# Performance work log

Measured on AMD Instinct MI355X. Metric: run time of the kernel, lower is better.

## Reference

```python
import jax, jax.numpy as jnp
import numpy as np

BETA = 0.5
THR = 1.0

@jax.custom_vjp
def spike(u):
    # heaviside fire; surrogate ATan gradient (snntorch default, alpha=2)
    return (u > 0.0).astype(u.dtype)

def _spike_fwd(u):
    return spike(u), u

def _spike_bwd(u, g):
    return (g / (1.0 + (jnp.pi * u) ** 2),)

spike.defvjp(_spike_fwd, _spike_bwd)

def setup_inputs() -> dict:
    key = jax.random.key(0)
    k = jax.random.split(key, 5)
    T, B, NI, NH, NO = 100, 65536, 2, 10, 4
    x = jax.random.normal(k[0], (T, B, NI), dtype=jnp.float32)
    # PyTorch Linear init: U(-1/sqrt(fan_in), 1/sqrt(fan_in))
    W1 = jax.random.uniform(k[1], (NH, NI), jnp.float32, -1/np.sqrt(NI), 1/np.sqrt(NI))
    b1 = jax.random.uniform(k[2], (NH,), jnp.float32, -1/np.sqrt(NI), 1/np.sqrt(NI))
    W2 = jax.random.uniform(k[3], (NO, NH), jnp.float32, -1/np.sqrt(NH), 1/np.sqrt(NH))
    b2 = jax.random.uniform(k[4], (NO,), jnp.float32, -1/np.sqrt(NH), 1/np.sqrt(NH))
    return {"x": x, "W1": W1, "b1": b1, "W2": W2, "b2": b2}

def _lif(mem_prev, syn):
    # snntorch Leaky, reset_mechanism='subtract':
    # reset computed from PRE-update membrane, detached
    reset = jax.lax.stop_gradient((mem_prev > THR).astype(syn.dtype))
    mem = BETA * mem_prev + syn - reset * THR
    spk = spike(mem - THR)
    return spk, mem

def reference(x, W1, b1, W2, b2):
    T, B = x.shape[0], x.shape[1]
    mem1_0 = jnp.zeros((B, W1.shape[0]), x.dtype)
    mem2_0 = jnp.zeros((B, W2.shape[0]), x.dtype)

    def step(carry, xt):
        mem1, mem2 = carry
        syn1 = xt @ W1.T + b1            # [B, NH]
        spk1, mem1 = _lif(mem1, syn1)
        syn2 = spk1 @ W2.T + b2          # [B, NO]
        spk2, mem2 = _lif(mem2, syn2)
        return (mem1, mem2), (spk1, mem1, spk2, mem2)

    _, (spk1_rec, mem1_rec, spk2_rec, mem2_rec) = jax.lax.scan(step, (mem1_0, mem2_0), x)
    return spk1_rec, mem1_rec, spk2_rec, mem2_rec
```

## Files before the change

### kernel.cpp

```cpp
#include <hip/hip_runtime.h>
#include <stdint.h>

#define T_STEPS 100
#define BATCH   65536
#define NI      2
#define NH      10
#define NO      4
#define KCH     10
#define TC      10

typedef float vf2 __attribute__((ext_vector_type(2)));
typedef float vf4 __attribute__((ext_vector_type(4)));

#define LOAD_WEIGHTS                                                        \
    float w1[NH][NI], bb1[NH], w2[NO][NH], bb2[NO];                         \
    _Pragma("unroll") for (int h = 0; h < NH; ++h) {                        \
        w1[h][0] = W1[h * NI + 0];                                          \
        w1[h][1] = W1[h * NI + 1];                                          \
        bb1[h]   = b1[h];                                                   \
    }                                                                       \
    _Pragma("unroll") for (int o = 0; o < NO; ++o) {                        \
        _Pragma("unroll") for (int h = 0; h < NH; ++h)                      \
            w2[o][h] = W2[o * NH + h];                                      \
        bb2[o] = b2[o];                                                     \
    }

__device__ __forceinline__ void lif_step(
    const float x0, const float x1,
    const float w1[NH][NI], const float bb1[NH],
    const float w2[NO][NH], const float bb2[NO],
    float m1[NH], float m2[NO], float spk1[NH], float spk2[NO])
{
#pragma unroll
    for (int h = 0; h < NH; ++h) {
        float syn   = __builtin_fmaf(x1, w1[h][1], x0 * w1[h][0]) + bb1[h];
        float reset = (m1[h] > 1.0f) ? 1.0f : 0.0f;
        float m     = 0.5f * m1[h] + syn;
        m           = m - reset;
        m1[h]       = m;
        spk1[h]     = ((m - 1.0f) > 0.0f) ? 1.0f : 0.0f;
    }
#pragma unroll
    for (int o = 0; o < NO; ++o) {
        float acc = spk1[0] * w2[o][0];
#pragma unroll
        for (int h = 1; h < NH; ++h) acc = __builtin_fmaf(spk1[h], w2[o][h], acc);
        float syn   = acc + bb2[o];
        float reset = (m2[o] > 1.0f) ? 1.0f : 0.0f;
        float m     = 0.5f * m2[o] + syn;
        m           = m - reset;
        m2[o]       = m;
        spk2[o]     = ((m - 1.0f) > 0.0f) ? 1.0f : 0.0f;
    }
}

__global__ __launch_bounds__(256, 1) void snn_ckpt(
    const float* __restrict__ x, const float* __restrict__ W1,
    const float* __restrict__ b1, const float* __restrict__ W2,
    const float* __restrict__ b2, float* __restrict__ out)
{
    const int b = blockIdx.x * 256 + threadIdx.x;
    LOAD_WEIGHTS;

    float m1[NH], m2[NO];
#pragma unroll
    for (int h = 0; h < NH; ++h) m1[h] = 0.0f;
#pragma unroll
    for (int o = 0; o < NO; ++o) m2[o] = 0.0f;

    const size_t sec = (size_t)T_STEPS * BATCH;
    float* o_mem1 = out + sec * NH;
    float* o_mem2 = out + 2 * sec * NH + sec * NO;

    const vf2* xp = (const vf2*)x + b;
    vf2 xb[TC];
#pragma unroll
    for (int j = 0; j < TC; ++j) xb[j] = xp[(size_t)j * BATCH];

    for (int tt = 0; tt < T_STEPS; tt += TC) {
#pragma unroll
        for (int j = 0; j < TC; ++j) {
            const int t = tt + j;
            const float x0 = xb[j].x;
            const float x1 = xb[j].y;
            if (t + TC < T_STEPS) xb[j] = xp[(size_t)(t + TC) * BATCH];

            float spk1[NH], spk2[NO];
            lif_step(x0, x1, w1, bb1, w2, bb2, m1, m2, spk1, spk2);

            if (j == TC - 1 && t + 1 < T_STEPS) {
                float* pm1 = o_mem1 + ((size_t)t * BATCH + b) * NH;
                vf2* q = (vf2*)pm1;
#pragma unroll
                for (int i = 0; i < NH / 2; ++i) {
                    vf2 v; v.x = m1[2 * i]; v.y = m1[2 * i + 1];
                    q[i] = v;
                }
                vf4 v2; v2.x = m2[0]; v2.y = m2[1]; v2.z = m2[2]; v2.w = m2[3];
                *(vf4*)(o_mem2 + ((size_t)t * BATCH + b) * NO) = v2;
            }
        }
    }
}

__global__ __launch_bounds__(256, 4) void snn_out(
    const float* __restrict__ x, const float* __restrict__ W1,
    const float* __restrict__ b1, const float* __restrict__ W2,
    const float* __restrict__ b2, float* __restrict__ out)
{
    const int tid  = threadIdx.x;
    const int nbb  = BATCH / 256;
    const int k    = blockIdx.x / nbb;
    const int bb   = blockIdx.x % nbb;
    const int b    = bb * 256 + tid;
    const int t0   = k * TC;
    const int w    = tid >> 6;
    const int lane = tid & 63;
    const int wb0  = bb * 256 + (w << 6);

    LOAD_WEIGHTS;

    const size_t sec = (size_t)T_STEPS * BATCH;
    float* o_spk1 = out;
    float* o_mem1 = out + sec * NH;
    float* o_spk2 = out + 2 * sec * NH;
    float* o_mem2 = out + 2 * sec * NH + sec * NO;

    const vf2* xp = (const vf2*)x + b;
    vf2 xb[TC];
#pragma unroll
    for (int j = 0; j < TC; ++j) xb[j] = xp[(size_t)(t0 + j) * BATCH];

    float m1[NH], m2[NO];
    if (k == 0) {
#pragma unroll
        for (int h = 0; h < NH; ++h) m1[h] = 0.0f;
#pragma unroll
        for (int o = 0; o < NO; ++o) m2[o] = 0.0f;
    } else {
        const float* pm1 = o_mem1 + ((size_t)(t0 - 1) * BATCH + b) * NH;
#pragma unroll
        for (int i = 0; i < NH / 2; ++i) {
            vf2 v = ((const vf2*)pm1)[i];
            m1[2 * i] = v.x; m1[2 * i + 1] = v.y;
        }
        vf4 v2 = *(const vf4*)(o_mem2 + ((size_t)(t0 - 1) * BATCH + b) * NO);
        m2[0] = v2.x; m2[1] = v2.y; m2[2] = v2.z; m2[3] = v2.w;
    }

    __shared__ vf4 stage[4][2][160];
    float* s_spk = (float*)&stage[w][0][0];
    float* s_mem = (float*)&stage[w][1][0];

#pragma unroll
    for (int j = 0; j < TC; ++j) {
        const int t = t0 + j;
        float spk1[NH], spk2[NO];
        lif_step(xb[j].x, xb[j].y, w1, bb1, w2, bb2, m1, m2, spk1, spk2);

        {
            vf2* qs = (vf2*)s_spk;
            vf2* qm = (vf2*)s_mem;
#pragma unroll
            for (int i = 0; i < NH / 2; ++i) {
                vf2 vs; vs.x = spk1[2 * i]; vs.y = spk1[2 * i + 1];
                vf2 vm; vm.x = m1[2 * i];   vm.y = m1[2 * i + 1];
                qs[lane * 5 + i] = vs;
                qm[lane * 5 + i] = vm;
            }
        }
        __builtin_amdgcn_wave_barrier();

        const bool storeMem = (j < TC - 1) || (k == KCH - 1);

        {
            float* g = o_spk1 + (size_t)t * BATCH * NH + (size_t)wb0 * NH;
            vf4* g4 = (vf4*)g;
            g4[lane]      = stage[w][0][lane];
            g4[64 + lane] = stage[w][0][64 + lane];
            ((vf2*)g)[256 + lane] = ((vf2*)s_spk)[256 + lane];
        }
        if (storeMem) {
            float* g = o_mem1 + (size_t)t * BATCH * NH + (size_t)wb0 * NH;
            vf4* g4 = (vf4*)g;
            g4[lane]      = stage[w][1][lane];
            g4[64 + lane] = stage[w][1][64 + lane];
            ((vf2*)g)[256 + lane] = ((vf2*)s_mem)[256 + lane];
        }
        __builtin_amdgcn_wave_barrier();

        {
            vf4 vs; vs.x = spk2[0]; vs.y = spk2[1]; vs.z = spk2[2]; vs.w = spk2[3];
            *(vf4*)(o_spk2 + ((size_t)t * BATCH + b) * NO) = vs;
            if (storeMem) {
                vf4 vm; vm.x = m2[0]; vm.y = m2[1]; vm.z = m2[2]; vm.w = m2[3];
                *(vf4*)(o_mem2 + ((size_t)t * BATCH + b) * NO) = vm;
            }
        }
    }
}

extern "C" void kernel_launch(void* const* d_in, const int* in_sizes, int n_in,
                              void* d_out, int out_size, void* d_ws, size_t ws_size,
                              hipStream_t stream) {
    const float* x  = (const float*)d_in[0];
    const float* W1 = (const float*)d_in[1];
    const float* b1 = (const float*)d_in[2];
    const float* W2 = (const float*)d_in[3];
    const float* b2 = (const float*)d_in[4];
    float* out = (float*)d_out;

    snn_ckpt<<<BATCH / 256, 256, 0, stream>>>(x, W1, b1, W2, b2, out);
    snn_out<<<(BATCH / 256) * KCH, 256, 0, stream>>>(x, W1, b1, W2, b2, out);
}
```

Baseline: 811.1 us.

## Overlap checkpoint pass with first output chunk and scalarize weight loads

Merges the serial checkpoint kernel with the chunk-0 output work into a single launch. Chunk 0 needs no checkpoint, so its heavy store traffic can run alongside the 100-step recurrence, and the remaining chunks launch afterwards. Weight loads now go through readfirstlane so they live in scalar registers, which frees vector registers. The merged kernel drops its launch bound from 1 to 2 blocks per CU, which may change register allocation for the long checkpoint loop.

```diff
diff --git a/kernel.cpp b/kernel.cpp
--- a/kernel.cpp
+++ b/kernel.cpp
@@ -12,17 +12,21 @@
 typedef float vf2 __attribute__((ext_vector_type(2)));
 typedef float vf4 __attribute__((ext_vector_type(4)));
 
+__device__ __forceinline__ float uload(const float* p) {
+    return __uint_as_float((uint32_t)__builtin_amdgcn_readfirstlane((int)__float_as_uint(*p)));
+}
+
 #define LOAD_WEIGHTS                                                        \
     float w1[NH][NI], bb1[NH], w2[NO][NH], bb2[NO];                         \
     _Pragma("unroll") for (int h = 0; h < NH; ++h) {                        \
-        w1[h][0] = W1[h * NI + 0];                                          \
-        w1[h][1] = W1[h * NI + 1];                                          \
-        bb1[h]   = b1[h];                                                   \
+        w1[h][0] = uload(&W1[h * NI + 0]);                                  \
+        w1[h][1] = uload(&W1[h * NI + 1]);                                  \
+        bb1[h]   = uload(&b1[h]);                                           \
     }                                                                       \
     _Pragma("unroll") for (int o = 0; o < NO; ++o) {                        \
         _Pragma("unroll") for (int h = 0; h < NH; ++h)                      \
-            w2[o][h] = W2[o * NH + h];                                      \
-        bb2[o] = b2[o];                                                     \
+            w2[o][h] = uload(&W2[o * NH + h]);                              \
+        bb2[o] = uload(&b2[o]);                                             \
     }
 
 __device__ __forceinline__ void lif_step(
@@ -54,14 +58,12 @@
     }
 }
 
-__global__ __launch_bounds__(256, 1) void snn_ckpt(
-    const float* __restrict__ x, const float* __restrict__ W1,
-    const float* __restrict__ b1, const float* __restrict__ W2,
-    const float* __restrict__ b2, float* __restrict__ out)
-{
-    const int b = blockIdx.x * 256 + threadIdx.x;
-    LOAD_WEIGHTS;
-
+__device__ __forceinline__ void ckpt_body(
+    const int b, const float* __restrict__ x,
+    const float w1[NH][NI], const float bb1[NH],
+    const float w2[NO][NH], const float bb2[NO],
+    float* __restrict__ out)
+{
     float m1[NH], m2[NO];
 #pragma unroll
     for (int h = 0; h < NH; ++h) m1[h] = 0.0f;
@@ -103,22 +105,18 @@
     }
 }
 
-__global__ __launch_bounds__(256, 4) void snn_out(
-    const float* __restrict__ x, const float* __restrict__ W1,
-    const float* __restrict__ b1, const float* __restrict__ W2,
-    const float* __restrict__ b2, float* __restrict__ out)
-{
-    const int tid  = threadIdx.x;
-    const int nbb  = BATCH / 256;
-    const int k    = blockIdx.x / nbb;
-    const int bb   = blockIdx.x % nbb;
+__device__ __forceinline__ void out_chunk(
+    const int k, const int bb, const int tid,
+    const float* __restrict__ x,
+    const float w1[NH][NI], const float bb1[NH],
+    const float w2[NO][NH], const float bb2[NO],
+    float* __restrict__ out)
+{
     const int b    = bb * 256 + tid;
     const int t0   = k * TC;
     const int w    = tid >> 6;
     const int lane = tid & 63;
     const int wb0  = bb * 256 + (w << 6);
-
-    LOAD_WEIGHTS;
 
     const size_t sec = (size_t)T_STEPS * BATCH;
     float* o_spk1 = out;
@@ -198,6 +196,30 @@
             }
         }
     }
+}
+
+__global__ __launch_bounds__(256, 2) void snn_front(
+    const float* __restrict__ x, const float* __restrict__ W1,
+    const float* __restrict__ b1, const float* __restrict__ W2,
+    const float* __restrict__ b2, float* __restrict__ out)
+{
+    LOAD_WEIGHTS;
+    if (blockIdx.x < BATCH / 256) {
+        ckpt_body(blockIdx.x * 256 + threadIdx.x, x, w1, bb1, w2, bb2, out);
+    } else {
+        out_chunk(0, blockIdx.x - BATCH / 256, threadIdx.x, x, w1, bb1, w2, bb2, out);
+    }
+}
+
+__global__ __launch_bounds__(256, 4) void snn_rest(
+    const float* __restrict__ x, const float* __restrict__ W1,
+    const float* __restrict__ b1, const float* __restrict__ W2,
+    const float* __restrict__ b2, float* __restrict__ out)
+{
+    LOAD_WEIGHTS;
+    const int nbb = BATCH / 256;
+    out_chunk(1 + blockIdx.x / nbb, blockIdx.x % nbb, threadIdx.x,
+              x, w1, bb1, w2, bb2, out);
 }
 
 extern "C" void kernel_launch(void* const* d_in, const int* in_sizes, int n_in,
@@ -210,6 +232,6 @@
     const float* b2 = (const float*)d_in[4];
     float* out = (float*)d_out;
 
-    snn_ckpt<<<BATCH / 256, 256, 0, stream>>>(x, W1, b1, W2, b2, out);
-    snn_out<<<(BATCH / 256) * KCH, 256, 0, stream>>>(x, W1, b1, W2, b2, out);
-}
+    snn_front<<<2 * (BATCH / 256), 256, 0, stream>>>(x, W1, b1, W2, b2, out);
+    snn_rest<<<(BATCH / 256) * (KCH - 1), 256, 0, stream>>>(x, W1, b1, W2, b2, out);
+}
```

Result: faster. 777.3 us, median of 2 (-4.2%).

## Merge checkpoint and output kernels by recomputing prefix state per chunk

Applied to the files above, without the earlier changes.

Drops the sequential checkpoint kernel. Each time-chunk block now recomputes the membrane recurrence from t=0 up to its chunk start, then emits that chunk's outputs. This removes a second launch, the checkpoint writes and reads, and the dependency between kernels. The cost is redundant compute that grows with chunk index (about 4.5x the recurrence work on average) and extra x reads. Weight loads are also made wave-uniform via readfirstlane so they can live in scalar registers.

```diff
diff --git a/kernel.cpp b/kernel.cpp
--- a/kernel.cpp
+++ b/kernel.cpp
@@ -12,17 +12,21 @@
 typedef float vf2 __attribute__((ext_vector_type(2)));
 typedef float vf4 __attribute__((ext_vector_type(4)));
 
+__device__ __forceinline__ float uload(const float* p) {
+    return __uint_as_float((uint32_t)__builtin_amdgcn_readfirstlane((int)__float_as_uint(*p)));
+}
+
 #define LOAD_WEIGHTS                                                        \
     float w1[NH][NI], bb1[NH], w2[NO][NH], bb2[NO];                         \
     _Pragma("unroll") for (int h = 0; h < NH; ++h) {                        \
-        w1[h][0] = W1[h * NI + 0];                                          \
-        w1[h][1] = W1[h * NI + 1];                                          \
-        bb1[h]   = b1[h];                                                   \
+        w1[h][0] = uload(&W1[h * NI + 0]);                                  \
+        w1[h][1] = uload(&W1[h * NI + 1]);                                  \
+        bb1[h]   = uload(&b1[h]);                                           \
     }                                                                       \
     _Pragma("unroll") for (int o = 0; o < NO; ++o) {                        \
         _Pragma("unroll") for (int h = 0; h < NH; ++h)                      \
-            w2[o][h] = W2[o * NH + h];                                      \
-        bb2[o] = b2[o];                                                     \
+            w2[o][h] = uload(&W2[o * NH + h]);                              \
+        bb2[o] = uload(&b2[o]);                                             \
     }
 
 __device__ __forceinline__ void lif_step(
@@ -54,71 +58,20 @@
     }
 }
 
-__global__ __launch_bounds__(256, 1) void snn_ckpt(
+__global__ __launch_bounds__(256, 4) void snn_all(
     const float* __restrict__ x, const float* __restrict__ W1,
     const float* __restrict__ b1, const float* __restrict__ W2,
     const float* __restrict__ b2, float* __restrict__ out)
 {
-    const int b = blockIdx.x * 256 + threadIdx.x;
     LOAD_WEIGHTS;
 
-    float m1[NH], m2[NO];
-#pragma unroll
-    for (int h = 0; h < NH; ++h) m1[h] = 0.0f;
-#pragma unroll
-    for (int o = 0; o < NO; ++o) m2[o] = 0.0f;
-
-    const size_t sec = (size_t)T_STEPS * BATCH;
-    float* o_mem1 = out + sec * NH;
-    float* o_mem2 = out + 2 * sec * NH + sec * NO;
-
-    const vf2* xp = (const vf2*)x + b;
-    vf2 xb[TC];
-#pragma unroll
-    for (int j = 0; j < TC; ++j) xb[j] = xp[(size_t)j * BATCH];
-
-    for (int tt = 0; tt < T_STEPS; tt += TC) {
-#pragma unroll
-        for (int j = 0; j < TC; ++j) {
-            const int t = tt + j;
-            const float x0 = xb[j].x;
-            const float x1 = xb[j].y;
-            if (t + TC < T_STEPS) xb[j] = xp[(size_t)(t + TC) * BATCH];
-
-            float spk1[NH], spk2[NO];
-            lif_step(x0, x1, w1, bb1, w2, bb2, m1, m2, spk1, spk2);
-
-            if (j == TC - 1 && t + 1 < T_STEPS) {
-                float* pm1 = o_mem1 + ((size_t)t * BATCH + b) * NH;
-                vf2* q = (vf2*)pm1;
-#pragma unroll
-                for (int i = 0; i < NH / 2; ++i) {
-                    vf2 v; v.x = m1[2 * i]; v.y = m1[2 * i + 1];
-                    q[i] = v;
-                }
-                vf4 v2; v2.x = m2[0]; v2.y = m2[1]; v2.z = m2[2]; v2.w = m2[3];
-                *(vf4*)(o_mem2 + ((size_t)t * BATCH + b) * NO) = v2;
-            }
-        }
-    }
-}
-
-__global__ __launch_bounds__(256, 4) void snn_out(
-    const float* __restrict__ x, const float* __restrict__ W1,
-    const float* __restrict__ b1, const float* __restrict__ W2,
-    const float* __restrict__ b2, float* __restrict__ out)
-{
     const int tid  = threadIdx.x;
-    const int nbb  = BATCH / 256;
-    const int k    = blockIdx.x / nbb;
-    const int bb   = blockIdx.x % nbb;
+    const int k    = blockIdx.x % KCH;
+    const int bb   = blockIdx.x / KCH;
     const int b    = bb * 256 + tid;
-    const int t0   = k * TC;
     const int w    = tid >> 6;
     const int lane = tid & 63;
     const int wb0  = bb * 256 + (w << 6);
-
-    LOAD_WEIGHTS;
 
     const size_t sec = (size_t)T_STEPS * BATCH;
     float* o_spk1 = out;
@@ -129,23 +82,21 @@
     const vf2* xp = (const vf2*)x + b;
     vf2 xb[TC];
 #pragma unroll
-    for (int j = 0; j < TC; ++j) xb[j] = xp[(size_t)(t0 + j) * BATCH];
+    for (int j = 0; j < TC; ++j) xb[j] = xp[(size_t)j * BATCH];
 
     float m1[NH], m2[NO];
-    if (k == 0) {
 #pragma unroll
-        for (int h = 0; h < NH; ++h) m1[h] = 0.0f;
+    for (int h = 0; h < NH; ++h) m1[h] = 0.0f;
 #pragma unroll
-        for (int o = 0; o < NO; ++o) m2[o] = 0.0f;
-    } else {
-        const float* pm1 = o_mem1 + ((size_t)(t0 - 1) * BATCH + b) * NH;
+    for (int o = 0; o < NO; ++o) m2[o] = 0.0f;
+
+    for (int tt = 0; tt < k * TC; tt += TC) {
 #pragma unroll
-        for (int i = 0; i < NH / 2; ++i) {
-            vf2 v = ((const vf2*)pm1)[i];
-            m1[2 * i] = v.x; m1[2 * i + 1] = v.y;
+        for (int j = 0; j < TC; ++j) {
+            float spk1[NH], spk2[NO];
+            lif_step(xb[j].x, xb[j].y, w1, bb1, w2, bb2, m1, m2, spk1, spk2);
+            xb[j] = xp[(size_t)(tt + TC + j) * BATCH];
         }
-        vf4 v2 = *(const vf4*)(o_mem2 + ((size_t)(t0 - 1) * BATCH + b) * NO);
-        m2[0] = v2.x; m2[1] = v2.y; m2[2] = v2.z; m2[3] = v2.w;
     }
 
     __shared__ vf4 stage[4][2][160];
@@ -154,7 +105,7 @@
 
 #pragma unroll
     for (int j = 0; j < TC; ++j) {
-        const int t = t0 + j;
+        const int t = k * TC + j;
         float spk1[NH], spk2[NO];
         lif_step(xb[j].x, xb[j].y, w1, bb1, w2, bb2, m1, m2, spk1, spk2);
 
@@ -171,8 +122,6 @@
         }
         __builtin_amdgcn_wave_barrier();
 
-        const bool storeMem = (j < TC - 1) || (k == KCH - 1);
-
         {
             float* g = o_spk1 + (size_t)t * BATCH * NH + (size_t)wb0 * NH;
             vf4* g4 = (vf4*)g;
@@ -180,7 +129,7 @@
             g4[64 + lane] = stage[w][0][64 + lane];
             ((vf2*)g)[256 + lane] = ((vf2*)s_spk)[256 + lane];
         }
-        if (storeMem) {
+        {
             float* g = o_mem1 + (size_t)t * BATCH * NH + (size_t)wb0 * NH;
             vf4* g4 = (vf4*)g;
             g4[lane]      = stage[w][1][lane];
@@ -191,11 +140,9 @@
 
         {
             vf4 vs; vs.x = spk2[0]; vs.y = spk2[1]; vs.z = spk2[2]; vs.w = spk2[3];
+            vf4 vm; vm.x = m2[0];   vm.y = m2[1];   vm.z = m2[2];   vm.w = m2[3];
             *(vf4*)(o_spk2 + ((size_t)t * BATCH + b) * NO) = vs;
-            if (storeMem) {
-                vf4 vm; vm.x = m2[0]; vm.y = m2[1]; vm.z = m2[2]; vm.w = m2[3];
-                *(vf4*)(o_mem2 + ((size_t)t * BATCH + b) * NO) = vm;
-            }
+            *(vf4*)(o_mem2 + ((size_t)t * BATCH + b) * NO) = vm;
         }
     }
 }
@@ -210,6 +157,5 @@
     const float* b2 = (const float*)d_in[4];
     float* out = (float*)d_out;
 
-    snn_ckpt<<<BATCH / 256, 256, 0, stream>>>(x, W1, b1, W2, b2, out);
-    snn_out<<<(BATCH / 256) * KCH, 256, 0, stream>>>(x, W1, b1, W2, b2, out);
+    snn_all<<<(BATCH / 256) * KCH, 256, 0, stream>>>(x, W1, b1, W2, b2, out);
 }
```

Measured after the change: 882.6 us. +8.8%, slower.
